# Performance work log

Measured on AMD Instinct MI355X. Metric: run time of the kernel, lower is better.

The kernel has to match this reference:

```python
import jax, jax.numpy as jnp
import numpy as np

N, E, D, H = 100000, 1000000, 64, 4
HD = D // H  # head dim
G = 64       # num graphs in batch
EPS = 1e-5
NEG_SLOPE = 0.2


def setup_inputs() -> dict:
    key = jax.random.key(0)
    ks = jax.random.split(key, 10)
    x = jax.random.normal(ks[0], (N, D), dtype=jnp.float32)
    edge_index = jax.random.randint(ks[1], (2, E), 0, N)
    batch = jnp.sort(jax.random.randint(ks[2], (N,), 0, G))
    s = 1.0 / np.sqrt(D)
    Wl = jax.random.uniform(ks[3], (D, D), jnp.float32, -s, s)   # lin_l (source)
    Wr = jax.random.uniform(ks[4], (D, D), jnp.float32, -s, s)   # lin_r (target)
    att = jax.random.uniform(ks[5], (H, HD), jnp.float32, -s, s)
    bias_gat = jnp.zeros((D,), jnp.float32)
    gn_weight = jnp.ones((D,), jnp.float32)
    gn_bias = jnp.zeros((D,), jnp.float32)
    gn_mean_scale = jnp.ones((D,), jnp.float32)
    return {"x": x, "edge_index": edge_index, "batch": batch, "Wl": Wl,
            "Wr": Wr, "att": att, "bias_gat": bias_gat, "gn_weight": gn_weight,
            "gn_bias": gn_bias, "gn_mean_scale": gn_mean_scale}


def _gatv2(x, src, dst, Wl, Wr, att, bias_gat):
    # per-node linear projections, reshaped to heads
    xl = (x @ Wl).reshape(N, H, HD)  # source features
    xr = (x @ Wr).reshape(N, H, HD)  # target features
    # per-edge attention logits: a^T LeakyReLU(xl_j + xr_i)
    e = xl[src] + xr[dst]                             # [E', H, HD]
    e = jnp.where(e >= 0, e, NEG_SLOPE * e)           # leaky_relu
    score = jnp.einsum('ehd,hd->eh', e, att)          # [E', H]
    # segment softmax over incoming edges of each dst node
    m = jax.ops.segment_max(score, dst, num_segments=N)   # [N, H]
    p = jnp.exp(score - m[dst])
    denom = jax.ops.segment_sum(p, dst, num_segments=N)   # [N, H]
    alpha = p / denom[dst]                                # [E', H]
    # weighted scatter-add aggregation of source features
    out = jax.ops.segment_sum(alpha[:, :, None] * xl[src], dst, num_segments=N)
    return out.reshape(N, D) + bias_gat


def _graph_norm(h, batch, weight, bias, mean_scale):
    cnt = jax.ops.segment_sum(jnp.ones((N,), h.dtype), batch, num_segments=G)
    cnt = jnp.maximum(cnt, 1.0)[:, None]                      # [G,1]
    mean = jax.ops.segment_sum(h, batch, num_segments=G) / cnt
    out = h - mean_scale * mean[batch]
    var = jax.ops.segment_sum(out * out, batch, num_segments=G) / cnt
    return weight * out / jnp.sqrt(var[batch] + EPS) + bias


def reference(x, edge_index, batch, Wl, Wr, att, bias_gat, gn_weight, gn_bias, gn_mean_scale):
    # eval mode: dropout / DropEdge are identity; pre_norm=False; res_proj=Identity
    loops = jnp.arange(N)
    src = jnp.concatenate([edge_index[0], loops])  # add self-loops (PyG default)
    dst = jnp.concatenate([edge_index[1], loops])
    h = _gatv2(x, src, dst, Wl, Wr, att, bias_gat)
    h = h + x                                       # identity residual
    h = jnp.where(h > 0, h, jnp.expm1(h))           # ELU
    h = _graph_norm(h, batch, gn_weight, gn_bias, gn_mean_scale)
    return h
```

## Files before the change

kernel.cpp:

```cpp
#include <hip/hip_runtime.h>
#include <hip/hip_bf16.h>
#include <math.h>

#define G_ 64
#define NEG_SLOPE 0.2f
#define EPS_ 1e-5f
#define BBITS 7
#define BSZ 128
#define CAP 2048
#define EPB 2048

typedef __attribute__((ext_vector_type(8))) unsigned short ushort8;
typedef __attribute__((ext_vector_type(8))) short bf16x8;
typedef __attribute__((ext_vector_type(4))) float f32x4;

#define DPP_ADD(t, ctrl)                                                   \
  do {                                                                     \
    int _p = __builtin_amdgcn_update_dpp(0, __float_as_int(t), (ctrl),     \
                                         0xf, 0xf, true);                  \
    (t) += __int_as_float(_p);                                             \
  } while (0)
#define REDUCE8(t)                                                         \
  do {                                                                     \
    DPP_ADD(t, 0xB1);                                                      \
    DPP_ADD(t, 0x4E);                                                      \
    DPP_ADD(t, 0x141);                                                     \
  } while (0)

__device__ __forceinline__ float leaky_(float e) {
  return 0.6f * e + 0.4f * fabsf(e);
}

__device__ __forceinline__ short f2bf(float f) {
  __hip_bfloat16 h = __float2bfloat16(f);
  return *reinterpret_cast<short*>(&h);
}

__global__ __launch_bounds__(64) void prepack_kernel(
    const float* __restrict__ Wl, const float* __restrict__ Wr,
    bf16x8* __restrict__ bpack) {
  const int lane = threadIdx.x;
  const int lrow = lane & 15;
  const int lgrp = lane >> 4;
#pragma unroll
  for (int ct = 0; ct < 8; ++ct) {
    const float* W = (ct < 4) ? Wl : Wr;
    const int col = ((ct & 3) * 16) + lrow;
#pragma unroll
    for (int kk = 0; kk < 2; ++kk) {
      const int kb = kk * 32 + lgrp * 8;
      bf16x8 f;
#pragma unroll
      for (int j = 0; j < 8; ++j) f[j] = f2bf(W[(kb + j) * 64 + col]);
      bpack[(ct * 2 + kk) * 64 + lane] = f;
    }
  }
}

__global__ __launch_bounds__(256) void proj_mfma_kernel(
    const float* __restrict__ x, const bf16x8* __restrict__ bpack,
    __hip_bfloat16* __restrict__ xlb, __hip_bfloat16* __restrict__ xrb,
    int n) {
  const int lane = threadIdx.x & 63;
  const int wv = threadIdx.x >> 6;
  const int rbase = blockIdx.x * 64 + wv * 16;
  const int lrow = lane & 15;
  const int lgrp = lane >> 4;

  bf16x8 bfrag[8][2];
#pragma unroll
  for (int ct = 0; ct < 8; ++ct)
#pragma unroll
    for (int kk = 0; kk < 2; ++kk)
      bfrag[ct][kk] = bpack[(ct * 2 + kk) * 64 + lane];

  bf16x8 afrag[2];
  const int r = rbase + lrow;
#pragma unroll
  for (int kk = 0; kk < 2; ++kk) {
    bf16x8 f;
    if (r < n) {
      const float4* p = (const float4*)(x + (size_t)r * 64 + kk * 32 + lgrp * 8);
      float4 u = p[0], v = p[1];
      f[0] = f2bf(u.x); f[1] = f2bf(u.y); f[2] = f2bf(u.z); f[3] = f2bf(u.w);
      f[4] = f2bf(v.x); f[5] = f2bf(v.y); f[6] = f2bf(v.z); f[7] = f2bf(v.w);
    } else {
      f = bf16x8{0, 0, 0, 0, 0, 0, 0, 0};
    }
    afrag[kk] = f;
  }

  f32x4 acc[8];
#pragma unroll
  for (int ct = 0; ct < 8; ++ct) acc[ct] = f32x4{0.f, 0.f, 0.f, 0.f};
#pragma unroll
  for (int ct = 0; ct < 8; ++ct)
#pragma unroll
    for (int kk = 0; kk < 2; ++kk)
      acc[ct] = __builtin_amdgcn_mfma_f32_16x16x32_bf16(
          afrag[kk], bfrag[ct][kk], acc[ct], 0, 0, 0);

#pragma unroll
  for (int ct = 0; ct < 8; ++ct) {
    __hip_bfloat16* dst = (ct < 4) ? xlb : xrb;
    const int c = ((ct & 3) * 16) + lrow;
#pragma unroll
    for (int j = 0; j < 4; ++j) {
      const int rr = rbase + lgrp * 4 + j;
      if (rr < n) dst[(size_t)rr * 64 + c] = __float2bfloat16(acc[ct][j]);
    }
  }
}

__global__ __launch_bounds__(256) void bucket_kernel(
    const int* __restrict__ esrc, const int* __restrict__ edst,
    int* __restrict__ bcnt, unsigned int* __restrict__ packed,
    int e, int nb) {
  __shared__ int cnt[800];
  __shared__ int base[800];
  const int t = threadIdx.x;
  const int e0 = blockIdx.x * EPB;
  const int e1 = (e0 + EPB) < e ? (e0 + EPB) : e;
  for (int b = t; b < nb; b += 256) cnt[b] = 0;
  __syncthreads();
  for (int i = e0 + t; i < e1; i += 256)
    atomicAdd(&cnt[edst[i] >> BBITS], 1);
  __syncthreads();
  for (int b = t; b < nb; b += 256) {
    int c = cnt[b];
    base[b] = c ? atomicAdd(&bcnt[b], c) : 0;
    cnt[b] = 0;
  }
  __syncthreads();
  for (int i = e0 + t; i < e1; i += 256) {
    int d = edst[i];
    int b = d >> BBITS;
    int pos = base[b] + atomicAdd(&cnt[b], 1);
    if (pos < CAP)
      packed[(size_t)b * CAP + pos] =
          ((unsigned)(d & (BSZ - 1)) << 17) | (unsigned)esrc[i];
  }
}

__global__ __launch_bounds__(256) void sort_kernel(
    unsigned int* __restrict__ packed, const int* __restrict__ bcnt,
    int2* __restrict__ nse, int n) {
  __shared__ unsigned int stage[CAP];
  __shared__ int cnt[BSZ];
  __shared__ int sc[BSZ];
  __shared__ int off[BSZ + 1];
  const int t = threadIdx.x;
  const int b = blockIdx.x;
  int ecnt = bcnt[b];
  if (ecnt > CAP) ecnt = CAP;
  for (int j = t; j < ecnt; j += 256) stage[j] = packed[(size_t)b * CAP + j];
  if (t < BSZ) cnt[t] = 0;
  __syncthreads();
  for (int j = t; j < ecnt; j += 256) atomicAdd(&cnt[stage[j] >> 17], 1);
  __syncthreads();
  if (t < BSZ) sc[t] = cnt[t];
  __syncthreads();
#pragma unroll
  for (int o = 1; o < BSZ; o <<= 1) {
    int v = 0;
    if (t < BSZ && t >= o) v = sc[t - o];
    __syncthreads();
    if (t < BSZ) sc[t] += v;
    __syncthreads();
  }
  if (t < BSZ) {
    off[t + 1] = sc[t];
    if (t == 0) off[0] = 0;
    cnt[t] = sc[t] - cnt[t];
  }
  __syncthreads();
  for (int j = t; j < ecnt; j += 256) {
    unsigned v = stage[j];
    int pos = atomicAdd(&cnt[v >> 17], 1);
    packed[(size_t)b * CAP + pos] = v & 0x1FFFF;
  }
  const int nodebase = b << BBITS;
  if (t < BSZ && nodebase + t < n) {
    int s = off[t];
    nse[nodebase + t] = make_int2(b * CAP + s, off[t + 1] - s);
  }
}

template <int NB>
__device__ __forceinline__ void burst_(
    const char* xbase, unsigned poff, int myedge, int half, int tot,
    float xr0, float xr1, float a0, float a1,
    float& acc0, float& acc1, float& den) {
  unsigned vv[NB];
#pragma unroll
  for (int j = 0; j < NB; ++j) {
    const int sa = __builtin_amdgcn_readlane(myedge, 2 * j);
    const int sb = __builtin_amdgcn_readlane(myedge, 2 * j + 1);
    const int s = half ? sb : sa;
    vv[j] = *(const unsigned*)(xbase + (((unsigned)s << 7) | poff));
  }
#pragma unroll
  for (int j = 0; j < NB; ++j) {
    const unsigned v = vv[j];
    const float l0 = __uint_as_float(v << 16);
    const float l1 = __uint_as_float(v & 0xFFFF0000u);
    float e0 = leaky_(l0 + xr0);
    float e1 = leaky_(l1 + xr1);
    float t = a0 * e0 + a1 * e1;
    REDUCE8(t);
    float p = exp2f(t);
    p = ((2 * j + half) < tot) ? p : 0.f;
    acc0 = fmaf(p, l0, acc0);
    acc1 = fmaf(p, l1, acc1);
    den += p;
  }
}

__global__ __launch_bounds__(256) void aggregate_kernel(
    const __hip_bfloat16* __restrict__ xlb,
    const __hip_bfloat16* __restrict__ xrb, const float* __restrict__ x,
    const float* __restrict__ att, const float* __restrict__ bias_gat,
    const int2* __restrict__ nse, const unsigned int* __restrict__ srt,
    __hip_bfloat16* __restrict__ hb, int n) {
  const int lane = threadIdx.x & 63;
  const int i = (blockIdx.x * blockDim.x + threadIdx.x) >> 6;
  if (i >= n) return;
  const int pos = lane & 31;
  const int half = lane >> 5;
  const float2 attp = ((const float2*)att)[pos];
  const float a0 = attp.x * 1.44269504f;
  const float a1 = attp.y * 1.44269504f;
  const unsigned xr_pk = ((const unsigned*)(xrb + (size_t)i * 64))[pos];
  const float xr0 = __uint_as_float(xr_pk << 16);
  const float xr1 = __uint_as_float(xr_pk & 0xFFFF0000u);
  int2 sd = nse[i];
  const int s0 = __builtin_amdgcn_readfirstlane(sd.x);
  const int deg = __builtin_amdgcn_readfirstlane(sd.y);
  const int tot = deg + 1;
  int myedge = i;
  if (lane > 0 && lane < tot) myedge = (int)srt[s0 + lane - 1];
  float acc0 = 0.f, acc1 = 0.f, den = 0.f;
  const char* xbase = (const char*)xlb;
  const unsigned poff = (unsigned)pos << 2;

  if (tot <= 8) {
    burst_<4>(xbase, poff, myedge, half, tot, xr0, xr1, a0, a1,
              acc0, acc1, den);
  } else {
    burst_<8>(xbase, poff, myedge, half, tot, xr0, xr1, a0, a1,
              acc0, acc1, den);
    const int kmax = tot < 64 ? tot : 64;
    for (int k = 16; k < kmax; k += 2) {
      const int sa = __builtin_amdgcn_readlane(myedge, k);
      const int sb = (k + 1 < kmax) ? __builtin_amdgcn_readlane(myedge, k + 1)
                                    : sa;
      const int s = half ? sb : sa;
      const unsigned v = *(const unsigned*)(xbase + (((unsigned)s << 7) | poff));
      const float l0 = __uint_as_float(v << 16);
      const float l1 = __uint_as_float(v & 0xFFFF0000u);
      float e0 = leaky_(l0 + xr0);
      float e1 = leaky_(l1 + xr1);
      float t = a0 * e0 + a1 * e1;
      REDUCE8(t);
      float p = exp2f(t);
      p = ((k + half) < kmax) ? p : 0.f;
      acc0 = fmaf(p, l0, acc0);
      acc1 = fmaf(p, l1, acc1);
      den += p;
    }
    for (int kk = 64; kk < tot; ++kk) {
      const int s = (int)srt[s0 + kk - 1];
      const unsigned v = *(const unsigned*)(xbase + (((unsigned)s << 7) | poff));
      const float l0 = __uint_as_float(v << 16);
      const float l1 = __uint_as_float(v & 0xFFFF0000u);
      float e0 = leaky_(l0 + xr0);
      float e1 = leaky_(l1 + xr1);
      float t = a0 * e0 + a1 * e1;
      REDUCE8(t);
      float p = exp2f(t);
      p = half ? 0.f : p;
      acc0 = fmaf(p, l0, acc0);
      acc1 = fmaf(p, l1, acc1);
      den += p;
    }
  }

  acc0 += __shfl_xor(acc0, 32);
  acc1 += __shfl_xor(acc1, 32);
  den += __shfl_xor(den, 32);
  if (half == 0) {
    const float inv = 1.f / den;
    const float2 xres = ((const float2*)(x + (size_t)i * 64))[pos];
    const float2 bb = ((const float2*)bias_gat)[pos];
    float h0 = fmaf(acc0, inv, bb.x) + xres.x;
    float h1 = fmaf(acc1, inv, bb.y) + xres.y;
    h0 = h0 > 0.f ? h0 : expm1f(h0);
    h1 = h1 > 0.f ? h1 : expm1f(h1);
    __hip_bfloat16 b0 = __float2bfloat16(h0);
    __hip_bfloat16 b1 = __float2bfloat16(h1);
    unsigned pk = ((unsigned)(*(unsigned short*)&b1) << 16) |
                  (unsigned)(*(unsigned short*)&b0);
    ((unsigned*)(hb + (size_t)i * 64))[pos] = pk;
  }
}

__global__ __launch_bounds__(256) void gsum2_kernel(
    const __hip_bfloat16* __restrict__ h, const int* __restrict__ batch,
    float* __restrict__ gsum, float* __restrict__ gsq,
    float* __restrict__ gcnt, int n) {
  const int lane = threadIdx.x & 63;
  const int wave = (blockIdx.x * blockDim.x + threadIdx.x) >> 6;
  const int nwaves = (gridDim.x * blockDim.x) >> 6;
  const int chunk = (n + nwaves - 1) / nwaves;
  const int start = wave * chunk;
  const int end = (start + chunk) < n ? (start + chunk) : n;
  float s1 = 0.f, s2 = 0.f, cntl = 0.f;
  int curg = -1;
  for (int i = start; i < end; ++i) {
    int g = batch[i];
    if (g != curg) {
      if (curg >= 0) {
        atomicAdd(&gsum[curg * 64 + lane], s1);
        atomicAdd(&gsq[curg * 64 + lane], s2);
        if (lane == 0) atomicAdd(&gcnt[curg], cntl);
      }
      curg = g; s1 = 0.f; s2 = 0.f; cntl = 0.f;
    }
    float hv = __bfloat162float(h[(size_t)i * 64 + lane]);
    s1 += hv;
    s2 += hv * hv;
    cntl += 1.f;
  }
  if (curg >= 0) {
    atomicAdd(&gsum[curg * 64 + lane], s1);
    atomicAdd(&gsq[curg * 64 + lane], s2);
    if (lane == 0) atomicAdd(&gcnt[curg], cntl);
  }
}

__global__ void stats_kernel(const float* __restrict__ gsum,
                             const float* __restrict__ gsq,
                             const float* __restrict__ gcnt,
                             const float* __restrict__ mscale,
                             const float* __restrict__ w,
                             float* __restrict__ msmean,
                             float* __restrict__ scale) {
  int i = blockIdx.x * blockDim.x + threadIdx.x;
  if (i < G_ * 64) {
    int dd = i & 63;
    float c = gcnt[i >> 6];
    c = c > 1.f ? c : 1.f;
    float mean = gsum[i] / c;
    float ms = mscale[dd];
    float var = gsq[i] / c - ms * (2.f - ms) * mean * mean;
    msmean[i] = ms * mean;
    scale[i] = w[dd] * rsqrtf(var + EPS_);
  }
}

__global__ __launch_bounds__(256) void out_kernel(
    const __hip_bfloat16* __restrict__ hb, const int* __restrict__ batch,
    const float* __restrict__ msmean, const float* __restrict__ scale,
    const float* __restrict__ bias, float* __restrict__ out, int n) {
  const int total8 = n * 8;
  for (int idx = blockIdx.x * blockDim.x + threadIdx.x; idx < total8;
       idx += gridDim.x * blockDim.x) {
    int i = idx >> 3, q = idx & 7;
    int g = batch[i];
    int base = g * 64 + q * 8;
    ushort8 hv8 = ((const ushort8*)hb)[idx];
    float r[8];
#pragma unroll
    for (int j = 0; j < 8; ++j) {
      float f = __uint_as_float(((unsigned)hv8[j]) << 16);
      r[j] = (f - msmean[base + j]) * scale[base + j] + bias[q * 8 + j];
    }
    float4 o0 = make_float4(r[0], r[1], r[2], r[3]);
    float4 o1 = make_float4(r[4], r[5], r[6], r[7]);
    ((float4*)out)[idx * 2] = o0;
    ((float4*)out)[idx * 2 + 1] = o1;
  }
}

extern "C" void kernel_launch(void* const* d_in, const int* in_sizes, int n_in,
                              void* d_out, int out_size, void* d_ws, size_t ws_size,
                              hipStream_t stream) {
  const float* x        = (const float*)d_in[0];
  const int*   eidx     = (const int*)d_in[1];
  const int*   batch    = (const int*)d_in[2];
  const float* Wl       = (const float*)d_in[3];
  const float* Wr       = (const float*)d_in[4];
  const float* att      = (const float*)d_in[5];
  const float* bias_gat = (const float*)d_in[6];
  const float* gw       = (const float*)d_in[7];
  const float* gb       = (const float*)d_in[8];
  const float* gms      = (const float*)d_in[9];
  const int N = in_sizes[0] / 64;
  const int E = in_sizes[1] / 2;
  const int* esrc = eidx;
  const int* edst = eidx + E;
  float* out = (float*)d_out;
  const int NB_ = (N + BSZ - 1) >> BBITS;

  char* wsp = (char*)d_ws;
  float* gsum   = (float*)wsp;                wsp += G_ * 64 * 4;
  float* gsq    = (float*)wsp;                wsp += G_ * 64 * 4;
  float* gcnt   = (float*)wsp;                wsp += G_ * 4;
  float* msmean = (float*)wsp;                wsp += G_ * 64 * 4;
  float* scale  = (float*)wsp;                wsp += G_ * 64 * 4;
  bf16x8* bpack = (bf16x8*)wsp;               wsp += 16 * 64 * 16;
  int*   bcnt   = (int*)wsp;                  wsp += (size_t)NB_ * 4;
  int2*  nse    = (int2*)wsp;                 wsp += (size_t)N * 8;
  unsigned int* packed = (unsigned int*)wsp;  wsp += (size_t)NB_ * CAP * 4;
  __hip_bfloat16* xlb = (__hip_bfloat16*)wsp; wsp += (size_t)N * 64 * 2;
  __hip_bfloat16* xrb = (__hip_bfloat16*)wsp; wsp += (size_t)N * 64 * 2;
  __hip_bfloat16* hb  = (__hip_bfloat16*)wsp; wsp += (size_t)N * 64 * 2;

  hipMemsetAsync(gsum, 0, (size_t)(2 * G_ * 64 + G_) * sizeof(float), stream);
  hipMemsetAsync(bcnt, 0, (size_t)NB_ * sizeof(int), stream);

  prepack_kernel<<<1, 64, 0, stream>>>(Wl, Wr, bpack);
  proj_mfma_kernel<<<(N + 63) / 64, 256, 0, stream>>>(x, bpack, xlb, xrb, N);

  const int ab = (E + EPB - 1) / EPB;
  bucket_kernel<<<ab, 256, 0, stream>>>(esrc, edst, bcnt, packed, E, NB_);
  sort_kernel<<<NB_, 256, 0, stream>>>(packed, bcnt, nse, N);

  aggregate_kernel<<<(N + 3) / 4, 256, 0, stream>>>(
      xlb, xrb, x, att, bias_gat, nse, packed, hb, N);

  gsum2_kernel<<<1024, 256, 0, stream>>>(hb, batch, gsum, gsq, gcnt, N);
  stats_kernel<<<(G_ * 64 + 255) / 256, 256, 0, stream>>>(gsum, gsq, gcnt, gms,
                                                          gw, msmean, scale);
  out_kernel<<<3125, 256, 0, stream>>>(hb, batch, msmean, scale, gb, out, N);
}
```

Measured before the change: 165.5 us.

## Process two nodes per wavefront in aggregation and fold init/stats kernels

The aggregate kernel now handles two destination nodes per wavefront, issuing both nodes' first 16 neighbor gathers back to back so more loads are in flight before the compute. The prepack kernel and the two memsets are merged into one init kernel, and the stats kernel is removed by recomputing mean and scale inside out_kernel. This cuts launch count and raises memory-level parallelism in the gather. In exchange it uses more registers, always gathers 16 edges even for low-degree nodes, and repeats the per-element stats arithmetic in the output pass.

After: 161.0 us. -2.7%, faster.

```diff
diff --git a/kernel.cpp b/kernel.cpp
--- a/kernel.cpp
+++ b/kernel.cpp
@@ -36,24 +36,34 @@
   return *reinterpret_cast<short*>(&h);
 }
 
-__global__ __launch_bounds__(64) void prepack_kernel(
+__global__ __launch_bounds__(256) void init_kernel(
     const float* __restrict__ Wl, const float* __restrict__ Wr,
-    bf16x8* __restrict__ bpack) {
-  const int lane = threadIdx.x;
-  const int lrow = lane & 15;
-  const int lgrp = lane >> 4;
-#pragma unroll
-  for (int ct = 0; ct < 8; ++ct) {
-    const float* W = (ct < 4) ? Wl : Wr;
-    const int col = ((ct & 3) * 16) + lrow;
-#pragma unroll
-    for (int kk = 0; kk < 2; ++kk) {
-      const int kb = kk * 32 + lgrp * 8;
-      bf16x8 f;
-#pragma unroll
-      for (int j = 0; j < 8; ++j) f[j] = f2bf(W[(kb + j) * 64 + col]);
-      bpack[(ct * 2 + kk) * 64 + lane] = f;
-    }
+    bf16x8* __restrict__ bpack, int* __restrict__ bcnt,
+    float* __restrict__ gzero, int nb) {
+  if (blockIdx.x == 0) {
+    const int lane = threadIdx.x;
+    if (lane < 64) {
+      const int lrow = lane & 15;
+      const int lgrp = lane >> 4;
+#pragma unroll
+      for (int ct = 0; ct < 8; ++ct) {
+        const float* W = (ct < 4) ? Wl : Wr;
+        const int col = ((ct & 3) * 16) + lrow;
+#pragma unroll
+        for (int kk = 0; kk < 2; ++kk) {
+          const int kb = kk * 32 + lgrp * 8;
+          bf16x8 f;
+#pragma unroll
+          for (int j = 0; j < 8; ++j) f[j] = f2bf(W[(kb + j) * 64 + col]);
+          bpack[(ct * 2 + kk) * 64 + lane] = f;
+        }
+      }
+    }
+  } else {
+    const int idx = (blockIdx.x - 1) * 256 + threadIdx.x;
+    const int stride = (gridDim.x - 1) * 256;
+    for (int j = idx; j < nb; j += stride) bcnt[j] = 0;
+    for (int j = idx; j < 2 * G_ * 64 + G_; j += stride) gzero[j] = 0.f;
   }
 }
 
@@ -186,36 +196,6 @@
   }
 }
 
-template <int NB>
-__device__ __forceinline__ void burst_(
-    const char* xbase, unsigned poff, int myedge, int half, int tot,
-    float xr0, float xr1, float a0, float a1,
-    float& acc0, float& acc1, float& den) {
-  unsigned vv[NB];
-#pragma unroll
-  for (int j = 0; j < NB; ++j) {
-    const int sa = __builtin_amdgcn_readlane(myedge, 2 * j);
-    const int sb = __builtin_amdgcn_readlane(myedge, 2 * j + 1);
-    const int s = half ? sb : sa;
-    vv[j] = *(const unsigned*)(xbase + (((unsigned)s << 7) | poff));
-  }
-#pragma unroll
-  for (int j = 0; j < NB; ++j) {
-    const unsigned v = vv[j];
-    const float l0 = __uint_as_float(v << 16);
-    const float l1 = __uint_as_float(v & 0xFFFF0000u);
-    float e0 = leaky_(l0 + xr0);
-    float e1 = leaky_(l1 + xr1);
-    float t = a0 * e0 + a1 * e1;
-    REDUCE8(t);
-    float p = exp2f(t);
-    p = ((2 * j + half) < tot) ? p : 0.f;
-    acc0 = fmaf(p, l0, acc0);
-    acc1 = fmaf(p, l1, acc1);
-    den += p;
-  }
-}
-
 __global__ __launch_bounds__(256) void aggregate_kernel(
     const __hip_bfloat16* __restrict__ xlb,
     const __hip_bfloat16* __restrict__ xrb, const float* __restrict__ x,
@@ -223,84 +203,182 @@
     const int2* __restrict__ nse, const unsigned int* __restrict__ srt,
     __hip_bfloat16* __restrict__ hb, int n) {
   const int lane = threadIdx.x & 63;
-  const int i = (blockIdx.x * blockDim.x + threadIdx.x) >> 6;
-  if (i >= n) return;
+  const int wv = (blockIdx.x * blockDim.x + threadIdx.x) >> 6;
+  const int iA = wv * 2;
+  if (iA >= n) return;
+  const int iB = (iA + 1 < n) ? iA + 1 : iA;
   const int pos = lane & 31;
   const int half = lane >> 5;
   const float2 attp = ((const float2*)att)[pos];
   const float a0 = attp.x * 1.44269504f;
   const float a1 = attp.y * 1.44269504f;
-  const unsigned xr_pk = ((const unsigned*)(xrb + (size_t)i * 64))[pos];
-  const float xr0 = __uint_as_float(xr_pk << 16);
-  const float xr1 = __uint_as_float(xr_pk & 0xFFFF0000u);
-  int2 sd = nse[i];
-  const int s0 = __builtin_amdgcn_readfirstlane(sd.x);
-  const int deg = __builtin_amdgcn_readfirstlane(sd.y);
-  const int tot = deg + 1;
-  int myedge = i;
-  if (lane > 0 && lane < tot) myedge = (int)srt[s0 + lane - 1];
-  float acc0 = 0.f, acc1 = 0.f, den = 0.f;
   const char* xbase = (const char*)xlb;
   const unsigned poff = (unsigned)pos << 2;
 
-  if (tot <= 8) {
-    burst_<4>(xbase, poff, myedge, half, tot, xr0, xr1, a0, a1,
-              acc0, acc1, den);
-  } else {
-    burst_<8>(xbase, poff, myedge, half, tot, xr0, xr1, a0, a1,
-              acc0, acc1, den);
-    const int kmax = tot < 64 ? tot : 64;
+  const unsigned xrpA = ((const unsigned*)(xrb + (size_t)iA * 64))[pos];
+  const unsigned xrpB = ((const unsigned*)(xrb + (size_t)iB * 64))[pos];
+  const float xrA0 = __uint_as_float(xrpA << 16);
+  const float xrA1 = __uint_as_float(xrpA & 0xFFFF0000u);
+  const float xrB0 = __uint_as_float(xrpB << 16);
+  const float xrB1 = __uint_as_float(xrpB & 0xFFFF0000u);
+
+  int2 sdA = nse[iA];
+  int2 sdB = nse[iB];
+  const int s0A = __builtin_amdgcn_readfirstlane(sdA.x);
+  const int totA = __builtin_amdgcn_readfirstlane(sdA.y) + 1;
+  const int s0B = __builtin_amdgcn_readfirstlane(sdB.x);
+  const int totB = __builtin_amdgcn_readfirstlane(sdB.y) + 1;
+
+  int edgeA = iA, edgeB = iB;
+  if (lane > 0 && lane < totA) edgeA = (int)srt[s0A + lane - 1];
+  if (lane > 0 && lane < totB) edgeB = (int)srt[s0B + lane - 1];
+
+  unsigned vvA[8], vvB[8];
+#pragma unroll
+  for (int j = 0; j < 8; ++j) {
+    const int sa = __builtin_amdgcn_readlane(edgeA, 2 * j);
+    const int sb = __builtin_amdgcn_readlane(edgeA, 2 * j + 1);
+    const int s = half ? sb : sa;
+    vvA[j] = *(const unsigned*)(xbase + (((unsigned)s << 7) | poff));
+  }
+#pragma unroll
+  for (int j = 0; j < 8; ++j) {
+    const int sa = __builtin_amdgcn_readlane(edgeB, 2 * j);
+    const int sb = __builtin_amdgcn_readlane(edgeB, 2 * j + 1);
+    const int s = half ? sb : sa;
+    vvB[j] = *(const unsigned*)(xbase + (((unsigned)s << 7) | poff));
+  }
+
+  float accA0 = 0.f, accA1 = 0.f, denA = 0.f;
+  float accB0 = 0.f, accB1 = 0.f, denB = 0.f;
+#pragma unroll
+  for (int j = 0; j < 8; ++j) {
+    {
+      const unsigned v = vvA[j];
+      const float l0 = __uint_as_float(v << 16);
+      const float l1 = __uint_as_float(v & 0xFFFF0000u);
+      float t = a0 * leaky_(l0 + xrA0) + a1 * leaky_(l1 + xrA1);
+      REDUCE8(t);
+      float p = exp2f(t);
+      p = ((2 * j + half) < totA) ? p : 0.f;
+      accA0 = fmaf(p, l0, accA0);
+      accA1 = fmaf(p, l1, accA1);
+      denA += p;
+    }
+    {
+      const unsigned v = vvB[j];
+      const float l0 = __uint_as_float(v << 16);
+      const float l1 = __uint_as_float(v & 0xFFFF0000u);
+      float t = a0 * leaky_(l0 + xrB0) + a1 * leaky_(l1 + xrB1);
+      REDUCE8(t);
+      float p = exp2f(t);
+      p = ((2 * j + half) < totB) ? p : 0.f;
+      accB0 = fmaf(p, l0, accB0);
+      accB1 = fmaf(p, l1, accB1);
+      denB += p;
+    }
+  }
+
+  if (totA > 16) {
+    const int kmax = totA < 64 ? totA : 64;
     for (int k = 16; k < kmax; k += 2) {
-      const int sa = __builtin_amdgcn_readlane(myedge, k);
-      const int sb = (k + 1 < kmax) ? __builtin_amdgcn_readlane(myedge, k + 1)
+      const int sa = __builtin_amdgcn_readlane(edgeA, k);
+      const int sb = (k + 1 < kmax) ? __builtin_amdgcn_readlane(edgeA, k + 1)
                                     : sa;
       const int s = half ? sb : sa;
       const unsigned v = *(const unsigned*)(xbase + (((unsigned)s << 7) | poff));
       const float l0 = __uint_as_float(v << 16);
       const float l1 = __uint_as_float(v & 0xFFFF0000u);
-      float e0 = leaky_(l0 + xr0);
-      float e1 = leaky_(l1 + xr1);
-      float t = a0 * e0 + a1 * e1;
+      float t = a0 * leaky_(l0 + xrA0) + a1 * leaky_(l1 + xrA1);
       REDUCE8(t);
       float p = exp2f(t);
       p = ((k + half) < kmax) ? p : 0.f;
-      acc0 = fmaf(p, l0, acc0);
-      acc1 = fmaf(p, l1, acc1);
-      den += p;
-    }
-    for (int kk = 64; kk < tot; ++kk) {
-      const int s = (int)srt[s0 + kk - 1];
+      accA0 = fmaf(p, l0, accA0);
+      accA1 = fmaf(p, l1, accA1);
+      denA += p;
+    }
+    for (int kk = 64; kk < totA; ++kk) {
+      const int s = (int)srt[s0A + kk - 1];
       const unsigned v = *(const unsigned*)(xbase + (((unsigned)s << 7) | poff));
       const float l0 = __uint_as_float(v << 16);
       const float l1 = __uint_as_float(v & 0xFFFF0000u);
-      float e0 = leaky_(l0 + xr0);
-      float e1 = leaky_(l1 + xr1);
-      float t = a0 * e0 + a1 * e1;
+      float t = a0 * leaky_(l0 + xrA0) + a1 * leaky_(l1 + xrA1);
       REDUCE8(t);
       float p = exp2f(t);
       p = half ? 0.f : p;
-      acc0 = fmaf(p, l0, acc0);
-      acc1 = fmaf(p, l1, acc1);
-      den += p;
-    }
-  }
-
-  acc0 += __shfl_xor(acc0, 32);
-  acc1 += __shfl_xor(acc1, 32);
-  den += __shfl_xor(den, 32);
+      accA0 = fmaf(p, l0, accA0);
+      accA1 = fmaf(p, l1, accA1);
+      denA += p;
+    }
+  }
+  if (totB > 16) {
+    const int kmax = totB < 64 ? totB : 64;
+    for (int k = 16; k < kmax; k += 2) {
+      const int sa = __builtin_amdgcn_readlane(edgeB, k);
+      const int sb = (k + 1 < kmax) ? __builtin_amdgcn_readlane(edgeB, k + 1)
+                                    : sa;
+      const int s = half ? sb : sa;
+      const unsigned v = *(const unsigned*)(xbase + (((unsigned)s << 7) | poff));
+      const float l0 = __uint_as_float(v << 16);
+      const float l1 = __uint_as_float(v & 0xFFFF0000u);
+      float t = a0 * leaky_(l0 + xrB0) + a1 * leaky_(l1 + xrB1);
+      REDUCE8(t);
+      float p = exp2f(t);
+      p = ((k + half) < kmax) ? p : 0.f;
+      accB0 = fmaf(p, l0, accB0);
+      accB1 = fmaf(p, l1, accB1);
+      denB += p;
+    }
+    for (int kk = 64; kk < totB; ++kk) {
+      const int s = (int)srt[s0B + kk - 1];
+      const unsigned v = *(const unsigned*)(xbase + (((unsigned)s << 7) | poff));
+      const float l0 = __uint_as_float(v << 16);
+      const float l1 = __uint_as_float(v & 0xFFFF0000u);
+      float t = a0 * leaky_(l0 + xrB0) + a1 * leaky_(l1 + xrB1);
+      REDUCE8(t);
+      float p = exp2f(t);
+      p = half ? 0.f : p;
+      accB0 = fmaf(p, l0, accB0);
+      accB1 = fmaf(p, l1, accB1);
+      denB += p;
+    }
+  }
+
+  accA0 += __shfl_xor(accA0, 32);
+  accA1 += __shfl_xor(accA1, 32);
+  denA += __shfl_xor(denA, 32);
+  accB0 += __shfl_xor(accB0, 32);
+  accB1 += __shfl_xor(accB1, 32);
+  denB += __shfl_xor(denB, 32);
   if (half == 0) {
-    const float inv = 1.f / den;
-    const float2 xres = ((const float2*)(x + (size_t)i * 64))[pos];
-    const float2 bb = ((const float2*)bias_gat)[pos];
-    float h0 = fmaf(acc0, inv, bb.x) + xres.x;
-    float h1 = fmaf(acc1, inv, bb.y) + xres.y;
-    h0 = h0 > 0.f ? h0 : expm1f(h0);
-    h1 = h1 > 0.f ? h1 : expm1f(h1);
-    __hip_bfloat16 b0 = __float2bfloat16(h0);
-    __hip_bfloat16 b1 = __float2bfloat16(h1);
-    unsigned pk = ((unsigned)(*(unsigned short*)&b1) << 16) |
-                  (unsigned)(*(unsigned short*)&b0);
-    ((unsigned*)(hb + (size_t)i * 64))[pos] = pk;
+    {
+      const float inv = 1.f / denA;
+      const float2 xres = ((const float2*)(x + (size_t)iA * 64))[pos];
+      const float2 bb = ((const float2*)bias_gat)[pos];
+      float h0 = fmaf(accA0, inv, bb.x) + xres.x;
+      float h1 = fmaf(accA1, inv, bb.y) + xres.y;
+      h0 = h0 > 0.f ? h0 : expm1f(h0);
+      h1 = h1 > 0.f ? h1 : expm1f(h1);
+      __hip_bfloat16 b0 = __float2bfloat16(h0);
+      __hip_bfloat16 b1 = __float2bfloat16(h1);
+      unsigned pk = ((unsigned)(*(unsigned short*)&b1) << 16) |
+                    (unsigned)(*(unsigned short*)&b0);
+      ((unsigned*)(hb + (size_t)iA * 64))[pos] = pk;
+    }
+    {
+      const float inv = 1.f / denB;
+      const float2 xres = ((const float2*)(x + (size_t)iB * 64))[pos];
+      const float2 bb = ((const float2*)bias_gat)[pos];
+      float h0 = fmaf(accB0, inv, bb.x) + xres.x;
+      float h1 = fmaf(accB1, inv, bb.y) + xres.y;
+      h0 = h0 > 0.f ? h0 : expm1f(h0);
+      h1 = h1 > 0.f ? h1 : expm1f(h1);
+      __hip_bfloat16 b0 = __float2bfloat16(h0);
+      __hip_bfloat16 b1 = __float2bfloat16(h1);
+      unsigned pk = ((unsigned)(*(unsigned short*)&b1) << 16) |
+                    (unsigned)(*(unsigned short*)&b0);
+      ((unsigned*)(hb + (size_t)iB * 64))[pos] = pk;
+    }
   }
 }
 
@@ -338,42 +416,31 @@
   }
 }
 
-__global__ void stats_kernel(const float* __restrict__ gsum,
-                             const float* __restrict__ gsq,
-                             const float* __restrict__ gcnt,
-                             const float* __restrict__ mscale,
-                             const float* __restrict__ w,
-                             float* __restrict__ msmean,
-                             float* __restrict__ scale) {
-  int i = blockIdx.x * blockDim.x + threadIdx.x;
-  if (i < G_ * 64) {
-    int dd = i & 63;
-    float c = gcnt[i >> 6];
-    c = c > 1.f ? c : 1.f;
-    float mean = gsum[i] / c;
-    float ms = mscale[dd];
-    float var = gsq[i] / c - ms * (2.f - ms) * mean * mean;
-    msmean[i] = ms * mean;
-    scale[i] = w[dd] * rsqrtf(var + EPS_);
-  }
-}
-
 __global__ __launch_bounds__(256) void out_kernel(
     const __hip_bfloat16* __restrict__ hb, const int* __restrict__ batch,
-    const float* __restrict__ msmean, const float* __restrict__ scale,
-    const float* __restrict__ bias, float* __restrict__ out, int n) {
+    const float* __restrict__ gsum, const float* __restrict__ gsq,
+    const float* __restrict__ gcnt, const float* __restrict__ mscale,
+    const float* __restrict__ w, const float* __restrict__ bias,
+    float* __restrict__ out, int n) {
   const int total8 = n * 8;
   for (int idx = blockIdx.x * blockDim.x + threadIdx.x; idx < total8;
        idx += gridDim.x * blockDim.x) {
     int i = idx >> 3, q = idx & 7;
     int g = batch[i];
+    float c = gcnt[g];
+    c = c > 1.f ? c : 1.f;
+    float inv = 1.f / c;
     int base = g * 64 + q * 8;
     ushort8 hv8 = ((const ushort8*)hb)[idx];
     float r[8];
 #pragma unroll
     for (int j = 0; j < 8; ++j) {
+      int dd = q * 8 + j;
+      float mean = gsum[base + j] * inv;
+      float ms = mscale[dd];
+      float var = gsq[base + j] * inv - ms * (2.f - ms) * mean * mean;
       float f = __uint_as_float(((unsigned)hv8[j]) << 16);
-      r[j] = (f - msmean[base + j]) * scale[base + j] + bias[q * 8 + j];
+      r[j] = (f - ms * mean) * (w[dd] * rsqrtf(var + EPS_)) + bias[dd];
     }
     float4 o0 = make_float4(r[0], r[1], r[2], r[3]);
     float4 o1 = make_float4(r[4], r[5], r[6], r[7]);
@@ -406,8 +473,6 @@
   float* gsum   = (float*)wsp;                wsp += G_ * 64 * 4;
   float* gsq    = (float*)wsp;                wsp += G_ * 64 * 4;
   float* gcnt   = (float*)wsp;                wsp += G_ * 4;
-  float* msmean = (float*)wsp;                wsp += G_ * 64 * 4;
-  float* scale  = (float*)wsp;                wsp += G_ * 64 * 4;
   bf16x8* bpack = (bf16x8*)wsp;               wsp += 16 * 64 * 16;
   int*   bcnt   = (int*)wsp;                  wsp += (size_t)NB_ * 4;
   int2*  nse    = (int2*)wsp;                 wsp += (size_t)N * 8;
@@ -416,21 +481,17 @@
   __hip_bfloat16* xrb = (__hip_bfloat16*)wsp; wsp += (size_t)N * 64 * 2;
   __hip_bfloat16* hb  = (__hip_bfloat16*)wsp; wsp += (size_t)N * 64 * 2;
 
-  hipMemsetAsync(gsum, 0, (size_t)(2 * G_ * 64 + G_) * sizeof(float), stream);
-  hipMemsetAsync(bcnt, 0, (size_t)NB_ * sizeof(int), stream);
-
-  prepack_kernel<<<1, 64, 0, stream>>>(Wl, Wr, bpack);
+  init_kernel<<<9, 256, 0, stream>>>(Wl, Wr, bpack, bcnt, gsum, NB_);
   proj_mfma_kernel<<<(N + 63) / 64, 256, 0, stream>>>(x, bpack, xlb, xrb, N);
 
   const int ab = (E + EPB - 1) / EPB;
   bucket_kernel<<<ab, 256, 0, stream>>>(esrc, edst, bcnt, packed, E, NB_);
   sort_kernel<<<NB_, 256, 0, stream>>>(packed, bcnt, nse, N);
 
-  aggregate_kernel<<<(N + 3) / 4, 256, 0, stream>>>(
+  aggregate_kernel<<<(N + 7) / 8, 256, 0, stream>>>(
       xlb, xrb, x, att, bias_gat, nse, packed, hb, N);
 
   gsum2_kernel<<<1024, 256, 0, stream>>>(hb, batch, gsum, gsq, gcnt, N);
-  stats_kernel<<<(G_ * 64 + 255) / 256, 256, 0, stream>>>(gsum, gsq, gcnt, gms,
-                                                          gw, msmean, scale);
-  out_kernel<<<3125, 256, 0, stream>>>(hb, batch, msmean, scale, gb, out, N);
-}
+  out_kernel<<<3125, 256, 0, stream>>>(hb, batch, gsum, gsq, gcnt, gms, gw,
+                                       gb, out, N);
+}
```
